# Performance work log

Hardware: AMD Instinct MI355X
Metric: run time of the kernel (lower is better)

The kernel has to match this reference:

```python
import jax, jax.numpy as jnp
import numpy as np

EXTENTS = (1, 2, 2)   # local half-window per (s, h, w) axis -> window 3x5x5 = 75
HEADS = 8
DIM_HEAD = 32
MASK_VALUE = -1e9


def unfold_axis(x, axis, size):
    # sliding windows of `size` along `axis` (stride 1), window dim appended last
    n = x.shape[axis] - size + 1
    idx = jnp.arange(n)[:, None] + jnp.arange(size)[None, :]
    out = jnp.take(x, idx, axis=axis)          # (..., n, size, ...)
    return jnp.moveaxis(out, axis + 1, -1)     # (..., n, ..., size)


def unfold3d(x, extents):
    # mimics torch x.unfold over dims 1,2,3; appends 3 window dims at the end
    for i in range(3):
        x = unfold_axis(x, i + 1, 2 * extents[i] + 1)
    return x


def local3d_attention(x, q, wq, wk, wv, wo, bo):
    b, s, h, w, dim = q.shape
    heads, dh = HEADS, DIM_HEAD
    inner = heads * dh
    scale = dh ** -0.5
    es, eh, ew = EXTENTS

    k = x @ wk.T                               # (b,s,h,w,inner)
    v = x @ wv.T
    qp = q @ wq.T

    pad_cfg = ((0, 0), (es, es), (eh, eh), (ew, ew), (0, 0))
    N = b * s * h * w
    # unfold -> (b,s,h,w,inner,ks,kh,kw); inner is head-major: (heads, dh)
    kwin = unfold3d(jnp.pad(k, pad_cfg), EXTENTS).reshape(N, heads, dh, -1)
    vwin = unfold3d(jnp.pad(v, pad_cfg), EXTENTS).reshape(N, heads, dh, -1)
    win = kwin.shape[-1]

    # mask: True where window position falls in the zero padding
    m = jnp.zeros((1, s, h, w), dtype=bool)
    m = jnp.pad(m, ((0, 0), (es, es), (eh, eh), (ew, ew)), constant_values=True)
    m = unfold3d(m, EXTENTS).reshape(s * h * w, win)
    m = jnp.tile(m, (b, 1))

    qn = qp.reshape(N, heads, dh)
    dots = jnp.einsum('nhd,nhdk->nhk', qn, kwin) * scale
    dots = jnp.where(m[:, None, :], MASK_VALUE, dots)
    attn = jax.nn.softmax(dots, axis=-1)
    out = jnp.einsum('nhk,nhdk->nhd', attn, vwin).reshape(b, s, h, w, inner)
    return out @ wo.T + bo                     # (b,s,h,w,dim)


def setup_inputs() -> dict:
    key = jax.random.key(0)
    ks = jax.random.split(key, 6)
    b, s, h, w, dim = 2, 8, 32, 16, 256
    inner = HEADS * DIM_HEAD
    sc_in = dim ** -0.5
    sc_out = inner ** -0.5
    return {
        'x': jax.random.normal(ks[0], (b, s, h, w, dim), jnp.float32),
        'q': jax.random.normal(ks[1], (b, s, h, w, dim), jnp.float32),
        'wq': jax.random.normal(ks[2], (inner, dim), jnp.float32) * sc_in,
        'wk': jax.random.normal(ks[3], (inner, dim), jnp.float32) * sc_in,
        'wv': jax.random.normal(ks[4], (inner, dim), jnp.float32) * sc_in,
        'wo': jax.random.normal(ks[5], (dim, inner), jnp.float32) * sc_out,
        'bo': jnp.zeros((dim,), jnp.float32),
    }


def reference(x, q, wq, wk, wv, wo, bo):
    return local3d_attention(x, q, wq, wk, wv, wo, bo)
```

## Files before the change

kernel.cpp:

```cpp
#include <hip/hip_runtime.h>
#include <hip/hip_bf16.h>
#include <math.h>

#define HEADS 8
#define DH 32
#define DIM 256
#define INNER 256
#define B_ 2
#define S_ 8
#define H_ 32
#define W_ 16
#define NTOK (B_*S_*H_*W_)

#define VHSTRIDE (512*32*16)

typedef _Float16 h16;
typedef h16 half8 __attribute__((ext_vector_type(8)));
typedef h16 half4 __attribute__((ext_vector_type(4)));
typedef float f32x4 __attribute__((ext_vector_type(4)));

#define QSCALE 0.17677669529663687f

#define GBM 128
#define GBN 64
#define GBK 32
#define GPITCH 40

__device__ __forceinline__ uint4 cvt8(const float4 a, const float4 b) {
    union { h16 h[8]; uint4 u; } p;
    p.h[0] = (h16)a.x; p.h[1] = (h16)a.y; p.h[2] = (h16)a.z; p.h[3] = (h16)a.w;
    p.h[4] = (h16)b.x; p.h[5] = (h16)b.y; p.h[6] = (h16)b.z; p.h[7] = (h16)b.w;
    return p.u;
}

template <bool A_F16, int OUT_MODE>
__device__ __forceinline__ void mfma_gemm_tile_t(
    const void* __restrict__ Av, const float* __restrict__ W,
    const float* __restrict__ bias, void* __restrict__ outv,
    int m0, int j0, float oscale, h16* aT, h16* bT)
{
    const int tid  = threadIdx.x;
    const int lane = tid & 63;
    const int wid  = tid >> 6;
    const int wr   = wid >> 1;
    const int wc   = wid & 1;
    const int r    = lane & 15;
    const int g    = lane >> 4;

    f32x4 acc[4][2];
    #pragma unroll
    for (int i = 0; i < 4; ++i)
        #pragma unroll
        for (int j = 0; j < 2; ++j)
            acc[i][j] = (f32x4){0.f, 0.f, 0.f, 0.f};

    const int arow  = tid >> 1;
    const int ahalf = (tid & 1) * 16;
    const int brow  = (tid & 127) >> 1;
    const bool doB  = tid < 128;

    for (int k0 = 0; k0 < DIM; k0 += GBK) {
        if constexpr (A_F16) {
            const h16* A = (const h16*)Av;
            const h16* src = A + (size_t)(m0 + arow) * DIM + k0 + ahalf;
            *(uint4*)(aT + arow * GPITCH + ahalf + 0) = *(const uint4*)(src + 0);
            *(uint4*)(aT + arow * GPITCH + ahalf + 8) = *(const uint4*)(src + 8);
        } else {
            const float* A = (const float*)Av;
            const float* src = A + (size_t)(m0 + arow) * DIM + k0 + ahalf;
            const float4 u0 = *(const float4*)(src + 0);
            const float4 u1 = *(const float4*)(src + 4);
            const float4 u2 = *(const float4*)(src + 8);
            const float4 u3 = *(const float4*)(src + 12);
            *(uint4*)(aT + arow * GPITCH + ahalf + 0) = cvt8(u0, u1);
            *(uint4*)(aT + arow * GPITCH + ahalf + 8) = cvt8(u2, u3);
        }
        if (doB) {
            const float* src = W + (size_t)(j0 + brow) * DIM + k0 + ahalf;
            const float4 u0 = *(const float4*)(src + 0);
            const float4 u1 = *(const float4*)(src + 4);
            const float4 u2 = *(const float4*)(src + 8);
            const float4 u3 = *(const float4*)(src + 12);
            *(uint4*)(bT + brow * GPITCH + ahalf + 0) = cvt8(u0, u1);
            *(uint4*)(bT + brow * GPITCH + ahalf + 8) = cvt8(u2, u3);
        }
        __syncthreads();

        half8 af[4], bf[2];
        #pragma unroll
        for (int fr = 0; fr < 4; ++fr)
            af[fr] = *(const half8*)(aT + (wr * 64 + fr * 16 + r) * GPITCH + g * 8);
        #pragma unroll
        for (int fc = 0; fc < 2; ++fc)
            bf[fc] = *(const half8*)(bT + (wc * 32 + fc * 16 + r) * GPITCH + g * 8);

        #pragma unroll
        for (int fr = 0; fr < 4; ++fr)
            #pragma unroll
            for (int fc = 0; fc < 2; ++fc)
                acc[fr][fc] = __builtin_amdgcn_mfma_f32_16x16x32_f16(
                    af[fr], bf[fc], acc[fr][fc], 0, 0, 0);
        __syncthreads();
    }

    #pragma unroll
    for (int fr = 0; fr < 4; ++fr) {
        #pragma unroll
        for (int fc = 0; fc < 2; ++fc) {
            const int col = j0 + wc * 32 + fc * 16 + r;
            const float badd = bias ? bias[col] : 0.f;
            if constexpr (OUT_MODE == 4) {
                const int hd = col >> 5, d = col & 31;
                const int rowb = m0 + wr * 64 + fr * 16 + g * 4;
                union { h16 h[4]; uint2 u; } p;
                #pragma unroll
                for (int i = 0; i < 4; ++i) p.h[i] = (h16)(acc[fr][fc][i] * oscale);
                h16* dst = (h16*)outv + ((size_t)hd * 512 + (rowb >> 4)) * 512
                           + d * 16 + (rowb & 15);
                *(uint2*)dst = p.u;
            } else if constexpr (OUT_MODE == 3) {
                const int hd = col >> 5, d = col & 31;
                #pragma unroll
                for (int i = 0; i < 4; ++i) {
                    const int row = m0 + wr * 64 + fr * 16 + g * 4 + i;
                    ((h16*)outv)[((size_t)hd * NTOK + row) * DH + d] =
                        (h16)(acc[fr][fc][i] * oscale);
                }
            } else {
                #pragma unroll
                for (int i = 0; i < 4; ++i) {
                    const int row = m0 + wr * 64 + fr * 16 + g * 4 + i;
                    ((float*)outv)[(size_t)row * INNER + col] =
                        acc[fr][fc][i] * oscale + badd;
                }
            }
        }
    }
}

__global__ __launch_bounds__(256) void proj_kernel(
    const float* __restrict__ x, const float* __restrict__ q,
    const float* __restrict__ wq, const float* __restrict__ wk,
    const float* __restrict__ wv, h16* __restrict__ qk, h16* __restrict__ vtb)
{
    __shared__ h16 aT[GBM * GPITCH];
    __shared__ h16 bT[GBN * GPITCH];

    const int seg = blockIdx.y >> 2;
    const int jt  = blockIdx.y & 3;
    const float* A = (seg == 0) ? q : x;
    const float* W = (seg == 0) ? wq : ((seg == 1) ? wk : wv);

    if (seg == 2) {
        mfma_gemm_tile_t<false, 4>(A, W, nullptr, vtb, blockIdx.x * GBM, jt * GBN,
                                   1.0f, aT, bT);
    } else {
        h16* outp = qk + (size_t)seg * HEADS * NTOK * DH;
        const float sc = (seg == 0) ? QSCALE : 1.0f;
        mfma_gemm_tile_t<false, 3>(A, W, nullptr, outp, blockIdx.x * GBM, jt * GBN,
                                   sc, aT, bT);
    }
}

__global__ __launch_bounds__(256, 3) void attn_kernel(
    const h16* __restrict__ qk, const h16* __restrict__ vtb, h16* __restrict__ ao)
{
    const int tid  = threadIdx.x;
    const int lane = tid & 63;
    const int wid  = __builtin_amdgcn_readfirstlane(tid >> 6);
    const int xr   = blockIdx.x;
    const int blk  = ((xr & 7) << 7) | (xr >> 3);
    const int gid  = blk * 4 + wid;
    const int head = gid & 7;
    const int r    = gid >> 3;
    const int h = r & 31, s = (r >> 5) & 7, b = r >> 8;
    const int n_base = r * 16;
    const int c = lane & 15, g = lane >> 4;

    const h16* qb = qk + (size_t)head * NTOK * DH;
    const h16* kb = qk + (size_t)(HEADS + head) * NTOK * DH;
    const h16* vb = vtb + (size_t)head * VHSTRIDE;

    int   tokb[16];
    float kill[16];
    #pragma unroll
    for (int t = 0; t < 16; ++t) {
        const int ds = t / 5, hh = t - 5 * ds;
        const int s2 = s + ds - 1;
        const int h2 = h + hh - 2;
        const bool inb = (t < 15) && ((unsigned)s2 < 8u) && ((unsigned)h2 < 32u);
        const int s2c = min(max(s2, 0), 7);
        const int h2c = min(max(h2, 0), 31);
        tokb[t] = ((b * 8 + s2c) * 32 + h2c) * 16;
        kill[t] = inb ? __builtin_inff() : -1e30f;
    }

    const half8 qf = *(const half8*)(qb + (size_t)(n_base + c) * DH + g * 8);

    f32x4 dots[16];
    #pragma unroll
    for (int t = 0; t < 16; ++t) {
        const half8 kf = *(const half8*)(kb + (size_t)(tokb[t] + c) * DH + g * 8);
        dots[t] = __builtin_amdgcn_mfma_f32_16x16x32_f16(
            kf, qf, (f32x4){0.f, 0.f, 0.f, 0.f}, 0, 0, 0);
    }

    union u2h4 { uint2 u2; half4 hv; } vpre[16];
    #pragma unroll
    for (int t = 0; t < 16; ++t) {
        const int bv = tokb[t] >> 4;
        vpre[t].u2 = *(const uint2*)(vb + (size_t)bv * 512 + c * 16 + 4 * g);
    }

    bool okw[4];
    #pragma unroll
    for (int i = 0; i < 4; ++i) {
        const int w2 = 4 * g + i;
        okw[i] = ((unsigned)(w2 - c + 2) <= 4u);
    }
    float mx = -1e30f;
    #pragma unroll
    for (int t = 0; t < 16; ++t) {
        const float kl = kill[t];
        #pragma unroll
        for (int i = 0; i < 4; ++i) {
            float dv = okw[i] ? dots[t][i] : -1e30f;
            dv = fminf(dv, kl);
            dots[t][i] = dv;
            mx = fmaxf(mx, dv);
        }
    }
    mx = fmaxf(mx, __shfl_xor(mx, 16));
    mx = fmaxf(mx, __shfl_xor(mx, 32));

    float sum = 0.f;
    int d0[16], d1[16];
    #pragma unroll
    for (int t = 0; t < 16; ++t) {
        const float e0v = __expf(dots[t][0] - mx);
        const float e1v = __expf(dots[t][1] - mx);
        const float e2v = __expf(dots[t][2] - mx);
        const float e3v = __expf(dots[t][3] - mx);
        sum += (e0v + e1v) + (e2v + e3v);
        union { h16 hh2[2]; int u; } p0, p1;
        p0.hh2[0] = (h16)e0v; p0.hh2[1] = (h16)e1v;
        p1.hh2[0] = (h16)e2v; p1.hh2[1] = (h16)e3v;
        d0[t] = p0.u; d1[t] = p1.u;
    }
    sum += __shfl_xor(sum, 16);
    sum += __shfl_xor(sum, 32);
    const float inv = 1.f / sum;

    float invq[4];
    #pragma unroll
    for (int i = 0; i < 4; ++i) invq[i] = __shfl(inv, 4 * g + i);

    f32x4 o0 = (f32x4){0.f,0.f,0.f,0.f};
    f32x4 o1 = (f32x4){0.f,0.f,0.f,0.f};
    #pragma unroll
    for (int t = 0; t < 16; ++t) {
        union { int u[2]; half4 hv; } pa;
        pa.u[0] = d0[t]; pa.u[1] = d1[t];

        const int bv = tokb[t] >> 4;
        union u2h4 v1;
        v1.u2 = *(const uint2*)(vb + (size_t)bv * 512 + (c + 16) * 16 + 4 * g);

        o0 = __builtin_amdgcn_mfma_f32_16x16x16f16(pa.hv, vpre[t].hv, o0, 0, 0, 0);
        o1 = __builtin_amdgcn_mfma_f32_16x16x16f16(pa.hv, v1.hv, o1, 0, 0, 0);
    }

    #pragma unroll
    for (int i = 0; i < 4; ++i) {
        const size_t row = (size_t)(n_base + 4 * g + i) * INNER + head * DH;
        ao[row + c]      = (h16)(o0[i] * invq[i]);
        ao[row + 16 + c] = (h16)(o1[i] * invq[i]);
    }
}

__global__ __launch_bounds__(256) void outproj_kernel(
    const h16* __restrict__ ao, const float* __restrict__ wo,
    const float* __restrict__ bo, float* __restrict__ out)
{
    __shared__ h16 aT[GBM * GPITCH];
    __shared__ h16 bT[GBN * GPITCH];
    mfma_gemm_tile_t<true, 0>(ao, wo, bo, out, blockIdx.x * GBM, blockIdx.y * GBN,
                              1.0f, aT, bT);
}

extern "C" void kernel_launch(void* const* d_in, const int* in_sizes, int n_in,
                              void* d_out, int out_size, void* d_ws, size_t ws_size,
                              hipStream_t stream) {
    const float* x  = (const float*)d_in[0];
    const float* q  = (const float*)d_in[1];
    const float* wq = (const float*)d_in[2];
    const float* wk = (const float*)d_in[3];
    const float* wv = (const float*)d_in[4];
    const float* wo = (const float*)d_in[5];
    const float* bo = (const float*)d_in[6];
    float* out = (float*)d_out;

    h16* qk  = (h16*)d_ws;
    h16* vtb = qk + (size_t)2 * HEADS * NTOK * DH;
    h16* ao  = vtb + (size_t)HEADS * VHSTRIDE;

    dim3 g1(NTOK / GBM, 12);
    proj_kernel<<<g1, 256, 0, stream>>>(x, q, wq, wk, wv, qk, vtb);

    attn_kernel<<<1024, 256, 0, stream>>>(qk, vtb, ao);

    dim3 g3(NTOK / GBM, INNER / GBN);
    outproj_kernel<<<g3, 256, 0, stream>>>(ao, wo, bo, out);
}
```

Baseline: 43.87 us.

## Split attention window across two waves with flash-style softmax merge

```diff
diff --git a/kernel.cpp b/kernel.cpp
--- a/kernel.cpp
+++ b/kernel.cpp
@@ -162,17 +162,22 @@
     }
 }
 
-__global__ __launch_bounds__(256, 3) void attn_kernel(
+__global__ __launch_bounds__(256, 4) void attn_kernel(
     const h16* __restrict__ qk, const h16* __restrict__ vtb, h16* __restrict__ ao)
 {
+    __shared__ float ms[4][2][16];
+    __shared__ float obuf[2][64][9];
+
     const int tid  = threadIdx.x;
     const int lane = tid & 63;
     const int wid  = __builtin_amdgcn_readfirstlane(tid >> 6);
     const int xr   = blockIdx.x;
-    const int blk  = ((xr & 7) << 7) | (xr >> 3);
-    const int gid  = blk * 4 + wid;
-    const int head = gid & 7;
-    const int r    = gid >> 3;
+    const int blk  = ((xr & 7) << 8) | (xr >> 3);
+    const int uidx = wid >> 1;
+    const int unit = blk * 2 + uidx;
+    const int half = wid & 1;
+    const int head = unit & 7;
+    const int r    = unit >> 3;
     const int h = r & 31, s = (r >> 5) & 7, b = r >> 8;
     const int n_base = r * 16;
     const int c = lane & 15, g = lane >> 4;
@@ -181,14 +186,15 @@
     const h16* kb = qk + (size_t)(HEADS + head) * NTOK * DH;
     const h16* vb = vtb + (size_t)head * VHSTRIDE;
 
-    int   tokb[16];
-    float kill[16];
-    #pragma unroll
-    for (int t = 0; t < 16; ++t) {
-        const int ds = t / 5, hh = t - 5 * ds;
+    int   tokb[8];
+    float kill[8];
+    #pragma unroll
+    for (int t = 0; t < 8; ++t) {
+        const int run = half * 8 + t;
+        const int ds = run / 5, hh = run - 5 * ds;
         const int s2 = s + ds - 1;
         const int h2 = h + hh - 2;
-        const bool inb = (t < 15) && ((unsigned)s2 < 8u) && ((unsigned)h2 < 32u);
+        const bool inb = (run < 15) && ((unsigned)s2 < 8u) && ((unsigned)h2 < 32u);
         const int s2c = min(max(s2, 0), 7);
         const int h2c = min(max(h2, 0), 31);
         tokb[t] = ((b * 8 + s2c) * 32 + h2c) * 16;
@@ -197,17 +203,17 @@
 
     const half8 qf = *(const half8*)(qb + (size_t)(n_base + c) * DH + g * 8);
 
-    f32x4 dots[16];
-    #pragma unroll
-    for (int t = 0; t < 16; ++t) {
+    f32x4 dots[8];
+    #pragma unroll
+    for (int t = 0; t < 8; ++t) {
         const half8 kf = *(const half8*)(kb + (size_t)(tokb[t] + c) * DH + g * 8);
         dots[t] = __builtin_amdgcn_mfma_f32_16x16x32_f16(
             kf, qf, (f32x4){0.f, 0.f, 0.f, 0.f}, 0, 0, 0);
     }
 
-    union u2h4 { uint2 u2; half4 hv; } vpre[16];
-    #pragma unroll
-    for (int t = 0; t < 16; ++t) {
+    union u2h4 { uint2 u2; half4 hv; } vpre[8];
+    #pragma unroll
+    for (int t = 0; t < 8; ++t) {
         const int bv = tokb[t] >> 4;
         vpre[t].u2 = *(const uint2*)(vb + (size_t)bv * 512 + c * 16 + 4 * g);
     }
@@ -220,7 +226,7 @@
     }
     float mx = -1e30f;
     #pragma unroll
-    for (int t = 0; t < 16; ++t) {
+    for (int t = 0; t < 8; ++t) {
         const float kl = kill[t];
         #pragma unroll
         for (int i = 0; i < 4; ++i) {
@@ -234,9 +240,9 @@
     mx = fmaxf(mx, __shfl_xor(mx, 32));
 
     float sum = 0.f;
-    int d0[16], d1[16];
-    #pragma unroll
-    for (int t = 0; t < 16; ++t) {
+    int d0[8], d1[8];
+    #pragma unroll
+    for (int t = 0; t < 8; ++t) {
         const float e0v = __expf(dots[t][0] - mx);
         const float e1v = __expf(dots[t][1] - mx);
         const float e2v = __expf(dots[t][2] - mx);
@@ -249,16 +255,16 @@
     }
     sum += __shfl_xor(sum, 16);
     sum += __shfl_xor(sum, 32);
-    const float inv = 1.f / sum;
-
-    float invq[4];
-    #pragma unroll
-    for (int i = 0; i < 4; ++i) invq[i] = __shfl(inv, 4 * g + i);
+
+    if (lane < 16) {
+        ms[wid][0][lane] = mx;
+        ms[wid][1][lane] = sum;
+    }
 
     f32x4 o0 = (f32x4){0.f,0.f,0.f,0.f};
     f32x4 o1 = (f32x4){0.f,0.f,0.f,0.f};
     #pragma unroll
-    for (int t = 0; t < 16; ++t) {
+    for (int t = 0; t < 8; ++t) {
         union { int u[2]; half4 hv; } pa;
         pa.u[0] = d0[t]; pa.u[1] = d1[t];
 
@@ -270,11 +276,33 @@
         o1 = __builtin_amdgcn_mfma_f32_16x16x16f16(pa.hv, v1.hv, o1, 0, 0, 0);
     }
 
-    #pragma unroll
-    for (int i = 0; i < 4; ++i) {
-        const size_t row = (size_t)(n_base + 4 * g + i) * INNER + head * DH;
-        ao[row + c]      = (h16)(o0[i] * invq[i]);
-        ao[row + 16 + c] = (h16)(o1[i] * invq[i]);
+    if (half == 1) {
+        #pragma unroll
+        for (int i = 0; i < 4; ++i) {
+            obuf[uidx][lane][i]     = o0[i];
+            obuf[uidx][lane][4 + i] = o1[i];
+        }
+    }
+    __syncthreads();
+
+    if (half == 0) {
+        #pragma unroll
+        for (int i = 0; i < 4; ++i) {
+            const int qi = 4 * g + i;
+            const float m_a = ms[wid][0][qi],     s_a = ms[wid][1][qi];
+            const float m_b = ms[wid | 1][0][qi], s_b = ms[wid | 1][1][qi];
+            const float m  = fmaxf(m_a, m_b);
+            const float ea = __expf(m_a - m);
+            const float eb = __expf(m_b - m);
+            const float den = 1.f / (s_a * ea + s_b * eb);
+            const float ob0 = obuf[uidx][lane][i];
+            const float ob1 = obuf[uidx][lane][4 + i];
+            const float r0 = (o0[i] * ea + ob0 * eb) * den;
+            const float r1 = (o1[i] * ea + ob1 * eb) * den;
+            const size_t row = (size_t)(n_base + qi) * INNER + head * DH;
+            ao[row + c]      = (h16)r0;
+            ao[row + 16 + c] = (h16)r1;
+        }
     }
 }
 
@@ -307,7 +335,7 @@
     dim3 g1(NTOK / GBM, 12);
     proj_kernel<<<g1, 256, 0, stream>>>(x, q, wq, wk, wv, qk, vtb);
 
-    attn_kernel<<<1024, 256, 0, stream>>>(qk, vtb, ao);
+    attn_kernel<<<2048, 256, 0, stream>>>(qk, vtb, ao);
 
     dim3 g3(NTOK / GBM, INNER / GBN);
     outproj_kernel<<<g3, 256, 0, stream>>>(ao, wo, bo, out);
```

New measurement: 44.63 us. About the same (+1.7%).

## Fuse output projection into attention kernel via LDS-staged per-row tile

Applied to the files above, without the earlier changes.

```diff
diff --git a/kernel.cpp b/kernel.cpp
--- a/kernel.cpp
+++ b/kernel.cpp
@@ -13,6 +13,7 @@
 #define NTOK (B_*S_*H_*W_)
 
 #define VHSTRIDE (512*32*16)
+#define AOP 264
 
 typedef _Float16 h16;
 typedef h16 half8 __attribute__((ext_vector_type(8)));
@@ -33,11 +34,11 @@
     return p.u;
 }
 
-template <bool A_F16, int OUT_MODE>
+template <int OUT_MODE>
 __device__ __forceinline__ void mfma_gemm_tile_t(
-    const void* __restrict__ Av, const float* __restrict__ W,
-    const float* __restrict__ bias, void* __restrict__ outv,
-    int m0, int j0, float oscale, h16* aT, h16* bT)
+    const float* __restrict__ A, const float* __restrict__ W,
+    void* __restrict__ outv, int m0, int j0, float oscale,
+    h16* aT, h16* bT)
 {
     const int tid  = threadIdx.x;
     const int lane = tid & 63;
@@ -60,13 +61,7 @@
     const bool doB  = tid < 128;
 
     for (int k0 = 0; k0 < DIM; k0 += GBK) {
-        if constexpr (A_F16) {
-            const h16* A = (const h16*)Av;
-            const h16* src = A + (size_t)(m0 + arow) * DIM + k0 + ahalf;
-            *(uint4*)(aT + arow * GPITCH + ahalf + 0) = *(const uint4*)(src + 0);
-            *(uint4*)(aT + arow * GPITCH + ahalf + 8) = *(const uint4*)(src + 8);
-        } else {
-            const float* A = (const float*)Av;
+        {
             const float* src = A + (size_t)(m0 + arow) * DIM + k0 + ahalf;
             const float4 u0 = *(const float4*)(src + 0);
             const float4 u1 = *(const float4*)(src + 4);
@@ -108,7 +103,6 @@
         #pragma unroll
         for (int fc = 0; fc < 2; ++fc) {
             const int col = j0 + wc * 32 + fc * 16 + r;
-            const float badd = bias ? bias[col] : 0.f;
             if constexpr (OUT_MODE == 4) {
                 const int hd = col >> 5, d = col & 31;
                 const int rowb = m0 + wr * 64 + fr * 16 + g * 4;
@@ -118,7 +112,7 @@
                 h16* dst = (h16*)outv + ((size_t)hd * 512 + (rowb >> 4)) * 512
                            + d * 16 + (rowb & 15);
                 *(uint2*)dst = p.u;
-            } else if constexpr (OUT_MODE == 3) {
+            } else {
                 const int hd = col >> 5, d = col & 31;
                 #pragma unroll
                 for (int i = 0; i < 4; ++i) {
@@ -126,13 +120,6 @@
                     ((h16*)outv)[((size_t)hd * NTOK + row) * DH + d] =
                         (h16)(acc[fr][fc][i] * oscale);
                 }
-            } else {
-                #pragma unroll
-                for (int i = 0; i < 4; ++i) {
-                    const int row = m0 + wr * 64 + fr * 16 + g * 4 + i;
-                    ((float*)outv)[(size_t)row * INNER + col] =
-                        acc[fr][fc][i] * oscale + badd;
-                }
             }
         }
     }
@@ -141,38 +128,50 @@
 __global__ __launch_bounds__(256) void proj_kernel(
     const float* __restrict__ x, const float* __restrict__ q,
     const float* __restrict__ wq, const float* __restrict__ wk,
-    const float* __restrict__ wv, h16* __restrict__ qk, h16* __restrict__ vtb)
+    const float* __restrict__ wv, const float* __restrict__ wo,
+    h16* __restrict__ qk, h16* __restrict__ vtb, h16* __restrict__ wof16)
 {
     __shared__ h16 aT[GBM * GPITCH];
     __shared__ h16 bT[GBN * GPITCH];
 
     const int seg = blockIdx.y >> 2;
     const int jt  = blockIdx.y & 3;
+
+    if (seg == 3) {
+        const int idx = (blockIdx.x * 256 + threadIdx.x) * 4;
+        const float4 v = *(const float4*)(wo + idx);
+        union { h16 h[4]; uint2 u; } p;
+        p.h[0] = (h16)v.x; p.h[1] = (h16)v.y;
+        p.h[2] = (h16)v.z; p.h[3] = (h16)v.w;
+        *(uint2*)(wof16 + idx) = p.u;
+        return;
+    }
+
     const float* A = (seg == 0) ? q : x;
     const float* W = (seg == 0) ? wq : ((seg == 1) ? wk : wv);
 
     if (seg == 2) {
-        mfma_gemm_tile_t<false, 4>(A, W, nullptr, vtb, blockIdx.x * GBM, jt * GBN,
-                                   1.0f, aT, bT);
+        mfma_gemm_tile_t<4>(A, W, vtb, blockIdx.x * GBM, jt * GBN, 1.0f, aT, bT);
     } else {
         h16* outp = qk + (size_t)seg * HEADS * NTOK * DH;
         const float sc = (seg == 0) ? QSCALE : 1.0f;
-        mfma_gemm_tile_t<false, 3>(A, W, nullptr, outp, blockIdx.x * GBM, jt * GBN,
-                                   sc, aT, bT);
-    }
-}
-
-__global__ __launch_bounds__(256, 3) void attn_kernel(
-    const h16* __restrict__ qk, const h16* __restrict__ vtb, h16* __restrict__ ao)
+        mfma_gemm_tile_t<3>(A, W, outp, blockIdx.x * GBM, jt * GBN, sc, aT, bT);
+    }
+}
+
+__global__ __launch_bounds__(512, 4) void attn_kernel(
+    const h16* __restrict__ qk, const h16* __restrict__ vtb,
+    const h16* __restrict__ wof16, const float* __restrict__ bo,
+    float* __restrict__ out)
 {
+    __shared__ h16 ao_lds[16][AOP];
+
     const int tid  = threadIdx.x;
     const int lane = tid & 63;
     const int wid  = __builtin_amdgcn_readfirstlane(tid >> 6);
     const int xr   = blockIdx.x;
-    const int blk  = ((xr & 7) << 7) | (xr >> 3);
-    const int gid  = blk * 4 + wid;
-    const int head = gid & 7;
-    const int r    = gid >> 3;
+    const int r    = ((xr & 7) << 6) | (xr >> 3);
+    const int head = wid;
     const int h = r & 31, s = (r >> 5) & 7, b = r >> 8;
     const int n_base = r * 16;
     const int c = lane & 15, g = lane >> 4;
@@ -250,7 +249,6 @@
     sum += __shfl_xor(sum, 16);
     sum += __shfl_xor(sum, 32);
     const float inv = 1.f / sum;
-
     float invq[4];
     #pragma unroll
     for (int i = 0; i < 4; ++i) invq[i] = __shfl(inv, 4 * g + i);
@@ -272,20 +270,35 @@
 
     #pragma unroll
     for (int i = 0; i < 4; ++i) {
-        const size_t row = (size_t)(n_base + 4 * g + i) * INNER + head * DH;
-        ao[row + c]      = (h16)(o0[i] * invq[i]);
-        ao[row + 16 + c] = (h16)(o1[i] * invq[i]);
-    }
-}
-
-__global__ __launch_bounds__(256) void outproj_kernel(
-    const h16* __restrict__ ao, const float* __restrict__ wo,
-    const float* __restrict__ bo, float* __restrict__ out)
-{
-    __shared__ h16 aT[GBM * GPITCH];
-    __shared__ h16 bT[GBN * GPITCH];
-    mfma_gemm_tile_t<true, 0>(ao, wo, bo, out, blockIdx.x * GBM, blockIdx.y * GBN,
-                              1.0f, aT, bT);
+        ao_lds[4 * g + i][head * DH + c]      = (h16)(o0[i] * invq[i]);
+        ao_lds[4 * g + i][head * DH + 16 + c] = (h16)(o1[i] * invq[i]);
+    }
+    __syncthreads();
+
+    const int n0 = wid * 32;
+    f32x4 oacc[2];
+    oacc[0] = (f32x4){0.f,0.f,0.f,0.f};
+    oacc[1] = (f32x4){0.f,0.f,0.f,0.f};
+    #pragma unroll
+    for (int kc = 0; kc < 8; ++kc) {
+        const half8 af = *(const half8*)&ao_lds[c][kc * 32 + g * 8];
+        #pragma unroll
+        for (int nt = 0; nt < 2; ++nt) {
+            const half8 bf = *(const half8*)(wof16
+                + (size_t)(n0 + nt * 16 + c) * DIM + kc * 32 + g * 8);
+            oacc[nt] = __builtin_amdgcn_mfma_f32_16x16x32_f16(af, bf, oacc[nt], 0, 0, 0);
+        }
+    }
+    #pragma unroll
+    for (int nt = 0; nt < 2; ++nt) {
+        const int col = n0 + nt * 16 + c;
+        const float badd = bo[col];
+        #pragma unroll
+        for (int i = 0; i < 4; ++i) {
+            const int row = n_base + 4 * g + i;
+            out[(size_t)row * INNER + col] = oacc[nt][i] + badd;
+        }
+    }
 }
 
 extern "C" void kernel_launch(void* const* d_in, const int* in_sizes, int n_in,
@@ -300,15 +313,12 @@
     const float* bo = (const float*)d_in[6];
     float* out = (float*)d_out;
 
-    h16* qk  = (h16*)d_ws;
-    h16* vtb = qk + (size_t)2 * HEADS * NTOK * DH;
-    h16* ao  = vtb + (size_t)HEADS * VHSTRIDE;
-
-    dim3 g1(NTOK / GBM, 12);
-    proj_kernel<<<g1, 256, 0, stream>>>(x, q, wq, wk, wv, qk, vtb);
-
-    attn_kernel<<<1024, 256, 0, stream>>>(qk, vtb, ao);
-
-    dim3 g3(NTOK / GBM, INNER / GBN);
-    outproj_kernel<<<g3, 256, 0, stream>>>(ao, wo, bo, out);
-}
+    h16* qk    = (h16*)d_ws;
+    h16* vtb   = qk + (size_t)2 * HEADS * NTOK * DH;
+    h16* wof16 = vtb + (size_t)HEADS * VHSTRIDE;
+
+    dim3 g1(NTOK / GBM, 13);
+    proj_kernel<<<g1, 256, 0, stream>>>(x, q, wq, wk, wv, wo, qk, vtb, wof16);
+
+    attn_kernel<<<512, 512, 0, stream>>>(qk, vtb, wof16, bo, out);
+}
```

After: 43.44 us. Within noise of the previous version (-1.0%).
